# Kernel tuning notes

Measured on AMD Instinct MI355X. Metric: run time of the kernel, lower is better.

Reference implementation:

```python
import jax, jax.numpy as jnp
import numpy as np

NUM_HEADS = 8
DIM_OUT = 768
SCALE = DIM_OUT ** (-0.5)


def setup_inputs() -> dict:
    key = jax.random.key(0)
    k1, k2, k3, k4, k5 = jax.random.split(key, 5)
    B, N1, N2, DIM_T, DIM_V, K = 4, 2048, 2048, 768, 1024, 4
    F_t = jax.random.normal(k1, (B, N1, DIM_T), dtype=jnp.float32)
    F_s = jax.random.normal(k2, (B, N2, DIM_V), dtype=jnp.float32)
    # stacked linear_proj weights, stored input-major: x @ W_lin[layer]
    W_lin = jax.random.normal(k3, (K, DIM_V, DIM_T), dtype=jnp.float32) * 0.02
    # conv1d(kernel=1) == pointwise linear, stored input-major: x @ W_q + b_q
    W_q = jax.random.normal(k4, (DIM_T, DIM_OUT), dtype=jnp.float32) * 0.02
    b_q = jax.random.normal(k5, (DIM_OUT,), dtype=jnp.float32) * 0.02
    layer = 1
    return {"F_t": F_t, "F_s": F_s, "W_lin": W_lin, "W_q": W_q, "b_q": b_q, "layer": layer}


def reference(F_t, F_s, W_lin, W_q, b_q, layer):
    B, N1, _ = F_t.shape
    N2 = F_s.shape[1]
    H = NUM_HEADS
    D = DIM_OUT // H  # head_dim

    # per-layer linear projection + L2 normalization of keys/values
    F_s_p = F_s @ W_lin[layer]                                   # [B,N2,dim_t]
    F_s_p = F_s_p / jnp.linalg.norm(F_s_p, axis=-1, keepdims=True)

    # conv1d kernel-size-1 Q projection == pointwise linear
    q = (F_t @ W_q + b_q).reshape(B, N1, H, D)                   # [B,N1,H,D]
    kv = F_s_p.reshape(B, N2, H, D)                              # [B,N2,H,D]

    attn = jnp.einsum('bnhd,bmhd->bhnm', q, kv) * SCALE          # [B,H,N1,N2]
    attn = jax.nn.softmax(attn, axis=-1)

    F_t_a = jnp.einsum('bhnm,bmhd->bnhd', attn, kv).reshape(B, N1, H * D)
    F_t_a = F_t_a + F_t                                          # residual
    F_t_a = F_t_a / jnp.linalg.norm(F_t_a, axis=-1, keepdims=True)
    return (F_t_a, F_s_p)
```

## Files before the change

### kernel.cpp

```cpp
#include <hip/hip_runtime.h>

using short8 = __attribute__((ext_vector_type(8))) short;
using f32x4  = __attribute__((ext_vector_type(4))) float;

#define DEV __device__ __forceinline__

#define GLBP(p) ((const __attribute__((address_space(1))) unsigned int*)(p))
#define LDSP(p) ((__attribute__((address_space(3))) unsigned int*)(p))

#define EXP2F(x) __builtin_amdgcn_exp2f(x)

DEV unsigned short f2bf(float f) {
    unsigned int u = __float_as_uint(f);
    u += 0x7fffu + ((u >> 16) & 1u);
    return (unsigned short)(u >> 16);
}

DEV unsigned int pack2bf(float a, float b) {
    unsigned int ua = __float_as_uint(a);
    ua += 0x7fffu + ((ua >> 16) & 1u);
    unsigned int ub = __float_as_uint(b);
    ub += 0x7fffu + ((ub >> 16) & 1u);
    return (ua >> 16) | (ub & 0xffff0000u);
}

__global__ __launch_bounds__(256) void wt_k(const float* __restrict__ in,
                                            unsigned short* __restrict__ out,
                                            int R, int C,
                                            const int* __restrict__ layerp, int lstride) {
    if (layerp) in += (size_t)layerp[0] * (size_t)lstride;
    __shared__ float t[32][33];
    const int tx = threadIdx.x & 31, ty = threadIdx.x >> 5;
    const int c0 = blockIdx.x * 32, r0 = blockIdx.y * 32;
#pragma unroll
    for (int it = 0; it < 4; ++it)
        t[ty + it * 8][tx] = in[(size_t)(r0 + ty + it * 8) * C + c0 + tx];
    __syncthreads();
#pragma unroll
    for (int it = 0; it < 4; ++it)
        out[(size_t)(c0 + ty + it * 8) * R + r0 + tx] = f2bf(t[tx][ty + it * 8]);
}

__global__ __launch_bounds__(256) void kvt_k(const unsigned short* __restrict__ kv,
                                             unsigned short* __restrict__ kvT) {
    const int n0 = blockIdx.x * 32, d0 = blockIdx.y * 32, bh = blockIdx.z;
    const int b = bh >> 3, h = bh & 7;
    __shared__ unsigned short t[32][33];
    const int tx = threadIdx.x & 31, ty = threadIdx.x >> 5;
#pragma unroll
    for (int it = 0; it < 4; ++it)
        t[ty + it * 8][tx] = kv[(size_t)(b * 2048 + n0 + ty + it * 8) * 768 + h * 96 + d0 + tx];
    __syncthreads();
#pragma unroll
    for (int it = 0; it < 4; ++it)
        kvT[((size_t)bh * 96 + d0 + ty + it * 8) * 2048 + n0 + tx] = t[tx][ty + it * 8];
}

template <int EPI, int AF32>
__global__ __launch_bounds__(256) void gemm128(const void* __restrict__ Av,
                                               const unsigned short* __restrict__ B,
                                               void* __restrict__ out,
                                               const float* __restrict__ bias,
                                               int K, int ldc, float oscale) {
    __shared__ unsigned short smA[4096];
    __shared__ unsigned short smB[3072];
    const int tid = threadIdx.x, lane = tid & 63;
    const int l15 = lane & 15, g = lane >> 4;
    const int w = tid >> 6, wm = w >> 1, wn = w & 1;
    const int m0 = blockIdx.x * 128, n0 = blockIdx.y * 96;
    const int srow = tid >> 2, skg = tid & 3;
    const int brow0 = tid % 96, bkg0 = tid / 96;
    const int c1 = tid + 256;
    const int brow1 = c1 % 96, bkg1 = c1 / 96;
    const unsigned short* pB0 = B + (size_t)(n0 + brow0) * K + bkg0 * 8;
    const unsigned short* pB1 = B + (size_t)(n0 + brow1) * K + bkg1 * 8;
    f32x4 acc[4][3] = {};
    const int nkt = K >> 5;
    for (int kt = 0; kt < nkt; ++kt) {
        const int k0 = kt << 5;
        __syncthreads();
        {
            __builtin_amdgcn_global_load_lds(GLBP(pB0 + k0), LDSP(smB + tid * 8), 16, 0, 0);
            if (tid < 128)
                __builtin_amdgcn_global_load_lds(GLBP(pB1 + k0), LDSP(smB + c1 * 8), 16, 0, 0);
            short8 va0, va1;
            if (AF32) {
                const float* A = (const float*)Av;
                const float* p0 = A + (size_t)(m0 + srow) * K + k0 + skg * 8;
                const float* p1 = A + (size_t)(m0 + 64 + srow) * K + k0 + skg * 8;
                float4 a0 = *(const float4*)p0, a0b = *(const float4*)(p0 + 4);
                float4 a1 = *(const float4*)p1, a1b = *(const float4*)(p1 + 4);
                va0[0] = f2bf(a0.x);  va0[1] = f2bf(a0.y);  va0[2] = f2bf(a0.z);  va0[3] = f2bf(a0.w);
                va0[4] = f2bf(a0b.x); va0[5] = f2bf(a0b.y); va0[6] = f2bf(a0b.z); va0[7] = f2bf(a0b.w);
                va1[0] = f2bf(a1.x);  va1[1] = f2bf(a1.y);  va1[2] = f2bf(a1.z);  va1[3] = f2bf(a1.w);
                va1[4] = f2bf(a1b.x); va1[5] = f2bf(a1b.y); va1[6] = f2bf(a1b.z); va1[7] = f2bf(a1b.w);
            } else {
                const unsigned short* A = (const unsigned short*)Av;
                va0 = *(const short8*)(A + (size_t)(m0 + srow) * K + k0 + skg * 8);
                va1 = *(const short8*)(A + (size_t)(m0 + 64 + srow) * K + k0 + skg * 8);
            }
            *(short8*)(smA + (skg * 128 + srow) * 8) = va0;
            *(short8*)(smA + (skg * 128 + 64 + srow) * 8) = va1;
        }
        __syncthreads();
        short8 af[4], bf[3];
#pragma unroll
        for (int i = 0; i < 4; ++i)
            af[i] = *(const short8*)(smA + (g * 128 + wm * 64 + i * 16 + l15) * 8);
#pragma unroll
        for (int j = 0; j < 3; ++j)
            bf[j] = *(const short8*)(smB + (g * 96 + wn * 48 + j * 16 + l15) * 8);
#pragma unroll
        for (int i = 0; i < 4; ++i)
#pragma unroll
            for (int j = 0; j < 3; ++j)
                acc[i][j] = __builtin_amdgcn_mfma_f32_16x16x32_bf16(af[i], bf[j], acc[i][j], 0, 0, 0);
    }
#pragma unroll
    for (int j = 0; j < 3; ++j) {
        const int col = n0 + wn * 48 + j * 16 + l15;
        const float bv = (EPI == 1) ? bias[col] : 0.0f;
#pragma unroll
        for (int i = 0; i < 4; ++i)
#pragma unroll
            for (int r = 0; r < 4; ++r) {
                const int row = m0 + wm * 64 + i * 16 + g * 4 + r;
                if (EPI == 0) {
                    ((float*)out)[(size_t)row * ldc + col] = acc[i][j][r];
                } else {
                    const float v = (acc[i][j][r] + bv) * oscale;
                    ((unsigned short*)out)[(size_t)row * ldc + col] = f2bf(v);
                }
            }
    }
}

__global__ __launch_bounds__(256) void rownorm_k(const float* __restrict__ in,
                                                 float* __restrict__ outf,
                                                 unsigned short* __restrict__ outb) {
    const int lane = threadIdx.x & 63;
    const int row = blockIdx.x * 4 + (threadIdx.x >> 6);
    const float* p = in + (size_t)row * 768;
    float4 v[3];
    float s = 0.f;
#pragma unroll
    for (int i = 0; i < 3; ++i) {
        v[i] = ((const float4*)p)[i * 64 + lane];
        s += v[i].x * v[i].x + v[i].y * v[i].y + v[i].z * v[i].z + v[i].w * v[i].w;
    }
#pragma unroll
    for (int mask = 1; mask < 64; mask <<= 1) s += __shfl_xor(s, mask);
    const float inv = rsqrtf(s);
    float4* of = (float4*)(outf + (size_t)row * 768);
    ushort4* ob = (ushort4*)(outb + (size_t)row * 768);
#pragma unroll
    for (int i = 0; i < 3; ++i) {
        float4 q;
        q.x = v[i].x * inv; q.y = v[i].y * inv; q.z = v[i].z * inv; q.w = v[i].w * inv;
        of[i * 64 + lane] = q;
        ushort4 u;
        u.x = f2bf(q.x); u.y = f2bf(q.y); u.z = f2bf(q.z); u.w = f2bf(q.w);
        ob[i * 64 + lane] = u;
    }
}

__global__ __launch_bounds__(256) void resid_norm_k(const float* __restrict__ in,
                                                    const float* __restrict__ res,
                                                    float* __restrict__ outf) {
    const int lane = threadIdx.x & 63;
    const int row = blockIdx.x * 4 + (threadIdx.x >> 6);
    const float4* pa = (const float4*)(in + (size_t)row * 768);
    const float4* pb = (const float4*)(res + (size_t)row * 768);
    float4 v[3];
    float s = 0.f;
#pragma unroll
    for (int i = 0; i < 3; ++i) {
        float4 a = pa[i * 64 + lane];
        float4 b = pb[i * 64 + lane];
        float4 c;
        c.x = a.x + b.x; c.y = a.y + b.y; c.z = a.z + b.z; c.w = a.w + b.w;
        v[i] = c;
        s += c.x * c.x + c.y * c.y + c.z * c.z + c.w * c.w;
    }
#pragma unroll
    for (int mask = 1; mask < 64; mask <<= 1) s += __shfl_xor(s, mask);
    const float inv = rsqrtf(s);
    float4* of = (float4*)(outf + (size_t)row * 768);
#pragma unroll
    for (int i = 0; i < 3; ++i) {
        float4 q;
        q.x = v[i].x * inv; q.y = v[i].y * inv; q.z = v[i].z * inv; q.w = v[i].w * inv;
        of[i * 64 + lane] = q;
    }
}

__global__ __launch_bounds__(512) void attn_k(const unsigned short* __restrict__ Q,
                                              const unsigned short* __restrict__ KV,
                                              const unsigned short* __restrict__ KVT,
                                              float* __restrict__ O) {
    __shared__ unsigned short sK[2][6144];
    __shared__ unsigned short sV[2][6144];
    __shared__ unsigned short plds[8][32][72];
    const int hw = blockIdx.x;
    const int bid = (hw & 7) * 32 + (hw >> 3);
    const int qb = bid & 7, h = (bid >> 3) & 7, b = bid >> 6;
    const int tid = threadIdx.x, lane = tid & 63, w = tid >> 6;
    const int l15 = lane & 15, g = lane >> 4;
    const int q0 = qb * 256 + w * 32;
    unsigned short(*pw)[72] = plds[w];

    const unsigned short* kb = KV + (size_t)(b * 2048) * 768 + h * 96;
    const unsigned short* vb = KVT + (size_t)((b * 8 + h) * 96) * 2048;

    const short8 kOnes = {(short)0x3F80, (short)0x3F80, (short)0x3F80, (short)0x3F80,
                          (short)0x3F80, (short)0x3F80, (short)0x3F80, (short)0x3F80};

    short8 aq[2][3];
#pragma unroll
    for (int mi = 0; mi < 2; ++mi) {
        const unsigned short* qp = Q + (size_t)(b * 2048 + q0 + mi * 16 + l15) * 768 + h * 96 + g * 8;
#pragma unroll
        for (int ks = 0; ks < 3; ++ks) aq[mi][ks] = *(const short8*)(qp + ks * 32);
    }
    f32x4 o[2][6] = {};
    f32x4 o6[2] = {};
    float m[2] = {-__builtin_inff(), -__builtin_inff()};

    const unsigned short* sgp[3];
    int sstep[3], soff[3], sisk[3];
#pragma unroll
    for (int p = 0; p < 3; ++p) {
        const int li = p * 8 + w;
        if (li < 12) {
            sgp[p] = kb + (size_t)lane * 768 + li * 8;
            sstep[p] = 64 * 768;
            soff[p] = li * 512;
            sisk[p] = 1;
        } else {
            const int j = li - 12;
            const int i = j * 64 + lane;
            const int kvsub = i / 96, d = i - kvsub * 96;
            sgp[p] = vb + (size_t)d * 2048 + kvsub * 8;
            sstep[p] = 64;
            soff[p] = j * 512;
            sisk[p] = 0;
        }
    }
    auto stage = [&](unsigned short* sKb, unsigned short* sVb) {
#pragma unroll
        for (int p = 0; p < 3; ++p) {
            __builtin_amdgcn_global_load_lds(GLBP(sgp[p]), LDSP((sisk[p] ? sKb : sVb) + soff[p]), 16, 0, 0);
            sgp[p] += sstep[p];
        }
    };

    stage(sK[0], sV[0]);
    __syncthreads();

    for (int c = 0; c < 32; ++c) {
        const int cur = c & 1;
        const unsigned short* sKb = sK[cur];
        const unsigned short* sVb = sV[cur];
        if (c < 31) stage(sK[cur ^ 1], sV[cur ^ 1]);

        f32x4 s[2][4];
        __builtin_amdgcn_s_setprio(1);
#pragma unroll
        for (int t = 0; t < 4; ++t) {
            short8 k0 = *(const short8*)(sKb + ((0 + g) * 64 + t * 16 + l15) * 8);
            short8 k1 = *(const short8*)(sKb + ((4 + g) * 64 + t * 16 + l15) * 8);
            short8 k2 = *(const short8*)(sKb + ((8 + g) * 64 + t * 16 + l15) * 8);
#pragma unroll
            for (int mi = 0; mi < 2; ++mi) {
                f32x4 a = {};
                a = __builtin_amdgcn_mfma_f32_16x16x32_bf16(k0, aq[mi][0], a, 0, 0, 0);
                a = __builtin_amdgcn_mfma_f32_16x16x32_bf16(k1, aq[mi][1], a, 0, 0, 0);
                a = __builtin_amdgcn_mfma_f32_16x16x32_bf16(k2, aq[mi][2], a, 0, 0, 0);
                s[mi][t] = a;
            }
        }
        __builtin_amdgcn_s_setprio(0);
#pragma unroll
        for (int mi = 0; mi < 2; ++mi) {
            float tm[4];
#pragma unroll
            for (int t = 0; t < 4; ++t)
                tm[t] = fmaxf(fmaxf(fmaxf(s[mi][t][0], s[mi][t][1]), s[mi][t][2]), s[mi][t][3]);
            float cm = fmaxf(fmaxf(fmaxf(tm[0], tm[1]), tm[2]), tm[3]);
            cm = fmaxf(cm, __shfl_xor(cm, 16));
            cm = fmaxf(cm, __shfl_xor(cm, 32));
            if (!__all(cm <= m[mi] + 11.5416f)) {
                const float nm = fmaxf(m[mi], cm);
                const float al = EXP2F(m[mi] - nm);
                m[mi] = nm;
                float alb[4];
#pragma unroll
                for (int r = 0; r < 4; ++r) alb[r] = __shfl(al, g * 4 + r);
#pragma unroll
                for (int dt = 0; dt < 6; ++dt)
#pragma unroll
                    for (int r = 0; r < 4; ++r) o[mi][dt][r] *= alb[r];
#pragma unroll
                for (int r = 0; r < 4; ++r) o6[mi][r] *= alb[r];
            }
#pragma unroll
            for (int t = 0; t < 4; ++t)
#pragma unroll
                for (int r = 0; r < 4; ++r)
                    s[mi][t][r] = EXP2F(s[mi][t][r] - m[mi]);
#pragma unroll
            for (int t = 0; t < 4; ++t) {
                uint2 pk;
                pk.x = pack2bf(s[mi][t][0], s[mi][t][1]);
                pk.y = pack2bf(s[mi][t][2], s[mi][t][3]);
                *(uint2*)&pw[mi * 16 + l15][t * 16 + g * 4] = pk;
            }
        }
        __builtin_amdgcn_s_setprio(1);
#pragma unroll
        for (int half = 0; half < 2; ++half) {
            short8 pa[2];
#pragma unroll
            for (int mi = 0; mi < 2; ++mi) {
                pa[mi] = *(const short8*)&pw[mi * 16 + l15][half * 32 + g * 8];
                o6[mi] = __builtin_amdgcn_mfma_f32_16x16x32_bf16(pa[mi], kOnes, o6[mi], 0, 0, 0);
            }
#pragma unroll
            for (int dt = 0; dt < 6; ++dt) {
                short8 bv = *(const short8*)(sVb + ((half * 4 + g) * 96 + dt * 16 + l15) * 8);
#pragma unroll
                for (int mi = 0; mi < 2; ++mi)
                    o[mi][dt] = __builtin_amdgcn_mfma_f32_16x16x32_bf16(pa[mi], bv, o[mi][dt], 0, 0, 0);
            }
        }
        __builtin_amdgcn_s_setprio(0);
        __syncthreads();
    }
#pragma unroll
    for (int mi = 0; mi < 2; ++mi)
#pragma unroll
        for (int r = 0; r < 4; ++r) {
            const float inv = 1.0f / o6[mi][r];
            float* op = O + (size_t)(b * 2048 + q0 + mi * 16 + g * 4 + r) * 768 + h * 96 + l15;
#pragma unroll
            for (int dt = 0; dt < 6; ++dt) op[dt * 16] = o[mi][dt][r] * inv;
        }
}

#define SCALE_F 0.05205877254075156f

extern "C" void kernel_launch(void* const* d_in, const int* in_sizes, int n_in,
                              void* d_out, int out_size, void* d_ws, size_t ws_size,
                              hipStream_t stream) {
    const float* Ft = (const float*)d_in[0];
    const float* Fs = (const float*)d_in[1];
    const float* Wl = (const float*)d_in[2];
    const float* Wq = (const float*)d_in[3];
    const float* bq = (const float*)d_in[4];
    const int* layer = (const int*)d_in[5];

    float* out0 = (float*)d_out;
    float* out1 = out0 + 6291456;

    char* ws = (char*)d_ws;
    unsigned short* wsQ   = (unsigned short*)(ws);
    unsigned short* wsWlt = (unsigned short*)(ws + 12582912);
    unsigned short* wsWqt = (unsigned short*)(ws + 14155776);
    unsigned short* wsKV  = (unsigned short*)(ws + 15335424);
    unsigned short* wsKVT = (unsigned short*)(ws + 27918336);
    float*          wsTmp = (float*)(ws + 40501248);

    wt_k<<<dim3(768 / 32, 1024 / 32), 256, 0, stream>>>(Wl, wsWlt, 1024, 768, layer, 1024 * 768);
    wt_k<<<dim3(768 / 32, 768 / 32), 256, 0, stream>>>(Wq, wsWqt, 768, 768, nullptr, 0);
    gemm128<0, 1><<<dim3(64, 8), 256, 0, stream>>>((const void*)Fs, wsWlt, (void*)wsTmp, nullptr, 1024, 768, 1.0f);
    rownorm_k<<<2048, 256, 0, stream>>>(wsTmp, out1, wsKV);
    kvt_k<<<dim3(64, 3, 32), 256, 0, stream>>>(wsKV, wsKVT);
    gemm128<1, 1><<<dim3(64, 8), 256, 0, stream>>>((const void*)Ft, wsWqt, (void*)wsQ, bq, 768, 768, SCALE_F);
    attn_k<<<256, 512, 0, stream>>>(wsQ, wsKV, wsKVT, wsTmp);
    resid_norm_k<<<2048, 256, 0, stream>>>(wsTmp, Ft, out0);
}
```

Baseline: 169.0 us.

## Merge weight transposes and projection GEMMs into single launches; store attention output as bf16

The two weight-transpose kernels are folded into one launch indexed by blockIdx.z, and so are the two projection GEMMs (K/V projection and Q projection). This removes two kernel launches and lets the two independent GEMMs fill the GPU together, doubling the grid for that stage. The attention output is now written as bf16 instead of fp32, and the residual/normalize kernel reads it back as bf16. That halves the bytes for this intermediate but adds rounding error before the residual add.

```diff
diff --git a/kernel.cpp b/kernel.cpp
--- a/kernel.cpp
+++ b/kernel.cpp
@@ -24,11 +24,25 @@
     return (ua >> 16) | (ub & 0xffff0000u);
 }
 
-__global__ __launch_bounds__(256) void wt_k(const float* __restrict__ in,
-                                            unsigned short* __restrict__ out,
-                                            int R, int C,
-                                            const int* __restrict__ layerp, int lstride) {
-    if (layerp) in += (size_t)layerp[0] * (size_t)lstride;
+__global__ __launch_bounds__(256) void wt2_k(const float* __restrict__ Wl,
+                                             const float* __restrict__ Wq,
+                                             unsigned short* __restrict__ outl,
+                                             unsigned short* __restrict__ outq,
+                                             const int* __restrict__ layerp) {
+    const int z = blockIdx.z;
+    int R, C;
+    const float* in;
+    unsigned short* out;
+    if (z == 0) {
+        R = 1024; C = 768;
+        in = Wl + (size_t)layerp[0] * (1024 * 768);
+        out = outl;
+    } else {
+        if (blockIdx.y >= 24) return;
+        R = 768; C = 768;
+        in = Wq;
+        out = outq;
+    }
     __shared__ float t[32][33];
     const int tx = threadIdx.x & 31, ty = threadIdx.x >> 5;
     const int c0 = blockIdx.x * 32, r0 = blockIdx.y * 32;
@@ -56,14 +70,20 @@
         kvT[((size_t)bh * 96 + d0 + ty + it * 8) * 2048 + n0 + tx] = t[tx][ty + it * 8];
 }
 
-template <int EPI, int AF32>
-__global__ __launch_bounds__(256) void gemm128(const void* __restrict__ Av,
-                                               const unsigned short* __restrict__ B,
-                                               void* __restrict__ out,
-                                               const float* __restrict__ bias,
-                                               int K, int ldc, float oscale) {
+__global__ __launch_bounds__(256) void gemm_dual(const float* __restrict__ A0,
+                                                 const unsigned short* __restrict__ B0,
+                                                 float* __restrict__ C0,
+                                                 const float* __restrict__ A1,
+                                                 const unsigned short* __restrict__ B1,
+                                                 unsigned short* __restrict__ C1,
+                                                 const float* __restrict__ bias,
+                                                 float oscale) {
     __shared__ unsigned short smA[4096];
     __shared__ unsigned short smB[3072];
+    const int z = blockIdx.z;
+    const float* A = z ? A1 : A0;
+    const unsigned short* B = z ? B1 : B0;
+    const int K = z ? 768 : 1024;
     const int tid = threadIdx.x, lane = tid & 63;
     const int l15 = lane & 15, g = lane >> 4;
     const int w = tid >> 6, wm = w >> 1, wn = w & 1;
@@ -83,22 +103,15 @@
             __builtin_amdgcn_global_load_lds(GLBP(pB0 + k0), LDSP(smB + tid * 8), 16, 0, 0);
             if (tid < 128)
                 __builtin_amdgcn_global_load_lds(GLBP(pB1 + k0), LDSP(smB + c1 * 8), 16, 0, 0);
+            const float* p0 = A + (size_t)(m0 + srow) * K + k0 + skg * 8;
+            const float* p1 = A + (size_t)(m0 + 64 + srow) * K + k0 + skg * 8;
+            float4 a0 = *(const float4*)p0, a0b = *(const float4*)(p0 + 4);
+            float4 a1 = *(const float4*)p1, a1b = *(const float4*)(p1 + 4);
             short8 va0, va1;
-            if (AF32) {
-                const float* A = (const float*)Av;
-                const float* p0 = A + (size_t)(m0 + srow) * K + k0 + skg * 8;
-                const float* p1 = A + (size_t)(m0 + 64 + srow) * K + k0 + skg * 8;
-                float4 a0 = *(const float4*)p0, a0b = *(const float4*)(p0 + 4);
-                float4 a1 = *(const float4*)p1, a1b = *(const float4*)(p1 + 4);
-                va0[0] = f2bf(a0.x);  va0[1] = f2bf(a0.y);  va0[2] = f2bf(a0.z);  va0[3] = f2bf(a0.w);
-                va0[4] = f2bf(a0b.x); va0[5] = f2bf(a0b.y); va0[6] = f2bf(a0b.z); va0[7] = f2bf(a0b.w);
-                va1[0] = f2bf(a1.x);  va1[1] = f2bf(a1.y);  va1[2] = f2bf(a1.z);  va1[3] = f2bf(a1.w);
-                va1[4] = f2bf(a1b.x); va1[5] = f2bf(a1b.y); va1[6] = f2bf(a1b.z); va1[7] = f2bf(a1b.w);
-            } else {
-                const unsigned short* A = (const unsigned short*)Av;
-                va0 = *(const short8*)(A + (size_t)(m0 + srow) * K + k0 + skg * 8);
-                va1 = *(const short8*)(A + (size_t)(m0 + 64 + srow) * K + k0 + skg * 8);
-            }
+            va0[0] = f2bf(a0.x);  va0[1] = f2bf(a0.y);  va0[2] = f2bf(a0.z);  va0[3] = f2bf(a0.w);
+            va0[4] = f2bf(a0b.x); va0[5] = f2bf(a0b.y); va0[6] = f2bf(a0b.z); va0[7] = f2bf(a0b.w);
+            va1[0] = f2bf(a1.x);  va1[1] = f2bf(a1.y);  va1[2] = f2bf(a1.z);  va1[3] = f2bf(a1.w);
+            va1[4] = f2bf(a1b.x); va1[5] = f2bf(a1b.y); va1[6] = f2bf(a1b.z); va1[7] = f2bf(a1b.w);
             *(short8*)(smA + (skg * 128 + srow) * 8) = va0;
             *(short8*)(smA + (skg * 128 + 64 + srow) * 8) = va1;
         }
@@ -119,17 +132,17 @@
 #pragma unroll
     for (int j = 0; j < 3; ++j) {
         const int col = n0 + wn * 48 + j * 16 + l15;
-        const float bv = (EPI == 1) ? bias[col] : 0.0f;
+        const float bv = z ? bias[col] : 0.0f;
 #pragma unroll
         for (int i = 0; i < 4; ++i)
 #pragma unroll
             for (int r = 0; r < 4; ++r) {
                 const int row = m0 + wm * 64 + i * 16 + g * 4 + r;
-                if (EPI == 0) {
-                    ((float*)out)[(size_t)row * ldc + col] = acc[i][j][r];
+                if (z == 0) {
+                    C0[(size_t)row * 768 + col] = acc[i][j][r];
                 } else {
                     const float v = (acc[i][j][r] + bv) * oscale;
-                    ((unsigned short*)out)[(size_t)row * ldc + col] = f2bf(v);
+                    C1[(size_t)row * 768 + col] = f2bf(v);
                 }
             }
     }
@@ -164,21 +177,24 @@
     }
 }
 
-__global__ __launch_bounds__(256) void resid_norm_k(const float* __restrict__ in,
+__global__ __launch_bounds__(256) void resid_norm_k(const unsigned short* __restrict__ in,
                                                     const float* __restrict__ res,
                                                     float* __restrict__ outf) {
     const int lane = threadIdx.x & 63;
     const int row = blockIdx.x * 4 + (threadIdx.x >> 6);
-    const float4* pa = (const float4*)(in + (size_t)row * 768);
+    const ushort4* pa = (const ushort4*)(in + (size_t)row * 768);
     const float4* pb = (const float4*)(res + (size_t)row * 768);
     float4 v[3];
     float s = 0.f;
 #pragma unroll
     for (int i = 0; i < 3; ++i) {
-        float4 a = pa[i * 64 + lane];
+        ushort4 a = pa[i * 64 + lane];
         float4 b = pb[i * 64 + lane];
         float4 c;
-        c.x = a.x + b.x; c.y = a.y + b.y; c.z = a.z + b.z; c.w = a.w + b.w;
+        c.x = __uint_as_float((unsigned int)a.x << 16) + b.x;
+        c.y = __uint_as_float((unsigned int)a.y << 16) + b.y;
+        c.z = __uint_as_float((unsigned int)a.z << 16) + b.z;
+        c.w = __uint_as_float((unsigned int)a.w << 16) + b.w;
         v[i] = c;
         s += c.x * c.x + c.y * c.y + c.z * c.z + c.w * c.w;
     }
@@ -197,7 +213,7 @@
 __global__ __launch_bounds__(512) void attn_k(const unsigned short* __restrict__ Q,
                                               const unsigned short* __restrict__ KV,
                                               const unsigned short* __restrict__ KVT,
-                                              float* __restrict__ O) {
+                                              unsigned short* __restrict__ O) {
     __shared__ unsigned short sK[2][6144];
     __shared__ unsigned short sV[2][6144];
     __shared__ unsigned short plds[8][32][72];
@@ -341,9 +357,9 @@
 #pragma unroll
         for (int r = 0; r < 4; ++r) {
             const float inv = 1.0f / o6[mi][r];
-            float* op = O + (size_t)(b * 2048 + q0 + mi * 16 + g * 4 + r) * 768 + h * 96 + l15;
-#pragma unroll
-            for (int dt = 0; dt < 6; ++dt) op[dt * 16] = o[mi][dt][r] * inv;
+            unsigned short* op = O + (size_t)(b * 2048 + q0 + mi * 16 + g * 4 + r) * 768 + h * 96 + l15;
+#pragma unroll
+            for (int dt = 0; dt < 6; ++dt) op[dt * 16] = f2bf(o[mi][dt][r] * inv);
         }
 }
 
@@ -369,13 +385,12 @@
     unsigned short* wsKV  = (unsigned short*)(ws + 15335424);
     unsigned short* wsKVT = (unsigned short*)(ws + 27918336);
     float*          wsTmp = (float*)(ws + 40501248);
-
-    wt_k<<<dim3(768 / 32, 1024 / 32), 256, 0, stream>>>(Wl, wsWlt, 1024, 768, layer, 1024 * 768);
-    wt_k<<<dim3(768 / 32, 768 / 32), 256, 0, stream>>>(Wq, wsWqt, 768, 768, nullptr, 0);
-    gemm128<0, 1><<<dim3(64, 8), 256, 0, stream>>>((const void*)Fs, wsWlt, (void*)wsTmp, nullptr, 1024, 768, 1.0f);
+    unsigned short* wsOb  = (unsigned short*)wsTmp;
+
+    wt2_k<<<dim3(24, 32, 2), 256, 0, stream>>>(Wl, Wq, wsWlt, wsWqt, layer);
+    gemm_dual<<<dim3(64, 8, 2), 256, 0, stream>>>(Fs, wsWlt, wsTmp, Ft, wsWqt, wsQ, bq, SCALE_F);
     rownorm_k<<<2048, 256, 0, stream>>>(wsTmp, out1, wsKV);
     kvt_k<<<dim3(64, 3, 32), 256, 0, stream>>>(wsKV, wsKVT);
-    gemm128<1, 1><<<dim3(64, 8), 256, 0, stream>>>((const void*)Ft, wsWqt, (void*)wsQ, bq, 768, 768, SCALE_F);
-    attn_k<<<256, 512, 0, stream>>>(wsQ, wsKV, wsKVT, wsTmp);
-    resid_norm_k<<<2048, 256, 0, stream>>>(wsTmp, Ft, out0);
-}
+    attn_k<<<256, 512, 0, stream>>>(wsQ, wsKV, wsKVT, wsOb);
+    resid_norm_k<<<2048, 256, 0, stream>>>(wsOb, Ft, out0);
+}
```

New measurement: 156.7 us. -7.3%, faster.
